# Performance work log

Measured on AMD Instinct MI355X. Metric: run time of the kernel, lower is better.

Reference implementation:

```python
import jax, jax.numpy as jnp
import numpy as np

N = 16384      # tokens
D_IN = 256     # input feature dim
D = 1024       # d_model
H = 2048       # expert hidden dim (2 * d_model)
E = 8          # n_experts
K = 2          # top_k
OUT = 2        # output classes
EPS = 1e-5


def layernorm(x, g, b):
    m = jnp.mean(x, axis=-1, keepdims=True)
    v = jnp.mean(jnp.square(x - m), axis=-1, keepdims=True)
    return (x - m) * jax.lax.rsqrt(v + EPS) * g + b


def setup_inputs() -> dict:
    key = jax.random.key(0)
    ks = jax.random.split(key, 10)
    s_in = 1.0 / np.sqrt(D_IN)
    s_d = 1.0 / np.sqrt(D)
    s_h = 1.0 / np.sqrt(H)
    return {
        "x": jax.random.normal(ks[0], (N, D_IN), jnp.float32),
        "w_in": jax.random.normal(ks[1], (D_IN, D), jnp.float32) * s_in,
        "b_in": jnp.zeros((D,), jnp.float32),
        "g_in": jnp.ones((D,), jnp.float32),
        "beta_in": jnp.zeros((D,), jnp.float32),
        "w_gate": jax.random.normal(ks[2], (D, E), jnp.float32) * s_d,
        "w1": jax.random.normal(ks[3], (E, D, H), jnp.float32) * s_d,
        "b1": jnp.zeros((E, H), jnp.float32),
        "w2": jax.random.normal(ks[4], (E, H, D), jnp.float32) * s_h,
        "b2": jnp.zeros((E, D), jnp.float32),
        "g_moe": jnp.ones((D,), jnp.float32),
        "beta_moe": jnp.zeros((D,), jnp.float32),
        "g_out": jnp.ones((D,), jnp.float32),
        "beta_out": jnp.zeros((D,), jnp.float32),
        "w_cls": jax.random.normal(ks[5], (D, OUT), jnp.float32) * s_d,
        "b_cls": jnp.zeros((OUT,), jnp.float32),
    }


def reference(x, w_in, b_in, g_in, beta_in, w_gate, w1, b1, w2, b2,
              g_moe, beta_moe, g_out, beta_out, w_cls, b_cls):
    # input projection + norm
    h = layernorm(x @ w_in + b_in, g_in, beta_in)            # [N, D]
    # router: softmax then top-k, renormalize over selected experts
    probs = jax.nn.softmax(h @ w_gate, axis=-1)              # [N, E]
    _, top_idx = jax.lax.top_k(probs, K)                     # [N, K]
    sel = jax.nn.one_hot(top_idx, E, dtype=probs.dtype).sum(axis=1)  # [N, E] 0/1
    gates = probs * sel
    gates = gates / (jnp.sum(gates, axis=-1, keepdims=True) + 1e-9)
    # experts: weighted combine; gate==0 tokens contribute nothing (same math
    # as the torch masked gather/scatter-add, dropout off in eval)
    mixed = jnp.zeros_like(h)
    for e in range(E):  # fixed, small expert count
        expert_out = jax.nn.gelu(h @ w1[e] + b1[e]) @ w2[e] + b2[e]  # [N, D]
        mixed = mixed + gates[:, e:e + 1] * expert_out
    out = layernorm(h + mixed, g_moe, beta_moe)
    out = layernorm(out, g_out, beta_out)
    return out @ w_cls + b_cls                               # [N, OUT]
```

## Files before the change

### kernel.cpp

```cpp
#include <hip/hip_runtime.h>
#include <hip/hip_bf16.h>

#define D_IN 256
#define DM   1024
#define HD   2048
#define NE   8
#define NTOK 16384

typedef __attribute__((ext_vector_type(8))) short short8;
typedef __attribute__((ext_vector_type(4))) float f32x4;
typedef unsigned int uint;

#define MT_TOFF1 0
#define MT_TOFF2 512
#define MT_CNT1  1536
#define MT_P1    1600
#define MT_OFF1  1664
#define MT_CNT2  1728
#define MT_PCNT2 1856
#define MT_TOTAL 1984

__device__ inline ushort f2bf(float v){
  __hip_bfloat16 b = __float2bfloat16(v);
  return *reinterpret_cast<ushort*>(&b);
}
__device__ inline float bf2f(ushort u){
  __hip_bfloat16 b = *reinterpret_cast<__hip_bfloat16*>(&u);
  return __bfloat162float(b);
}

__device__ inline float gelu_fast(float x){
  float u = 0.7978845608028654f * x * (1.0f + 0.044715f*x*x);
  return x / (1.0f + __expf(-2.0f*u));
}

__device__ inline void gload16(const void* g, void* l){
  __builtin_amdgcn_global_load_lds(
      (const __attribute__((address_space(1))) void*)g,
      (__attribute__((address_space(3))) void*)l, 16, 0, 0);
}


__global__ __launch_bounds__(256) void transpose_bf16_kernel(
    const float* __restrict__ src, ushort* __restrict__ dst, int R, int C)
{
  __shared__ float tile[32][33];
  int e = blockIdx.z;
  src += (size_t)e*R*C; dst += (size_t)e*R*C;
  int c0 = blockIdx.x*32, r0 = blockIdx.y*32;
  int tx = threadIdx.x & 31, ty = threadIdx.x >> 5;
  #pragma unroll
  for (int rr = ty; rr < 32; rr += 8)
    tile[rr][tx] = src[(size_t)(r0+rr)*C + c0+tx];
  __syncthreads();
  #pragma unroll
  for (int rr = ty; rr < 32; rr += 8)
    dst[(size_t)(c0+rr)*R + r0+tx] = f2bf(tile[tx][rr]);
}

__global__ __launch_bounds__(256) void split_x_kernel(
    const float* __restrict__ x, ushort* __restrict__ xs3)
{
  int g = blockIdx.x*256 + threadIdx.x;
  int e0 = g*4;
  int row = e0 >> 8, col = e0 & 255;
  f32x4 v = *(const f32x4*)(x + (size_t)row*D_IN + col);
  ushort4 hi, mi, lo;
  #pragma unroll
  for (int i=0;i<4;++i){
    float f = v[i];
    ushort h = f2bf(f);       float fh = bf2f(h);
    ushort m = f2bf(f - fh);  float fm = bf2f(m);
    ushort l = f2bf(f - fh - fm);
    ((ushort*)&hi)[i]=h; ((ushort*)&mi)[i]=m; ((ushort*)&lo)[i]=l;
  }
  ushort* base = xs3 + (size_t)row*768 + col;
  *(ushort4*)(base)       = hi;
  *(ushort4*)(base + 256) = mi;
  *(ushort4*)(base + 512) = lo;
}

__global__ __launch_bounds__(256) void transpose_split3_kernel(
    const float* __restrict__ src, ushort* __restrict__ dst)
{
  __shared__ float tile[32][33];
  int c0 = blockIdx.x*32, r0 = blockIdx.y*32;
  int tx = threadIdx.x & 31, ty = threadIdx.x >> 5;
  #pragma unroll
  for (int rr = ty; rr < 32; rr += 8)
    tile[rr][tx] = src[(size_t)(r0+rr)*DM + c0+tx];
  __syncthreads();
  #pragma unroll
  for (int rr = ty; rr < 32; rr += 8){
    float f = tile[tx][rr];
    ushort h = f2bf(f);       float fh = bf2f(h);
    ushort m = f2bf(f - fh);  float fm = bf2f(m);
    ushort l = f2bf(f - fh - fm);
    ushort* d = dst + (size_t)(c0+rr)*768 + r0 + tx;
    d[0]   = h;
    d[256] = m;
    d[512] = l;
  }
}

__global__ __launch_bounds__(256) void wgate_t_kernel(
    const float* __restrict__ w_gate, float* __restrict__ wgt)
{
  int e = blockIdx.x;
  for (int j = threadIdx.x; j < DM; j += 256)
    wgt[(size_t)e*DM + j] = w_gate[(size_t)j*NE + e];
}

__global__ __launch_bounds__(256) void gemm_router(
    const ushort* __restrict__ A,
    const ushort* __restrict__ BT,
    const float* __restrict__ b_in,
    float* __restrict__ y)
{
  __shared__ ushort As[3][128*32];
  __shared__ ushort Bs[3][128*32];
  const int tid = threadIdx.x;
  const int w = tid>>6, l = tid&63;
  const int wm = w>>1, wn = w&1;
  const int bm0 = blockIdx.y*128, bn0 = blockIdx.x*128;
  const int lr = l&15, lk = l>>4;
  const int rsub = l>>2;
  const int csub = ((l&3) ^ ((l>>3)&3)) * 8;

  const ushort* ag[2]; const ushort* bg[2];
  int aslot[2];
  #pragma unroll
  for (int i=0;i<2;++i){
    int ra = bm0 + w*32 + i*16 + rsub;
    int rb = bn0 + w*32 + i*16 + rsub;
    ag[i] = A  + (size_t)ra*768 + csub;
    bg[i] = BT + (size_t)rb*768 + csub;
    aslot[i] = (w*32 + i*16)*32;
  }

  const int pOffT[6] = {0,256,0,256,512,0};
  const int qOffT[6] = {0,0,256,256,0,512};
  auto stage = [&](int db, int t){
    int pOff = pOffT[t>>3] + (t&7)*32;
    int qOff = qOffT[t>>3] + (t&7)*32;
    #pragma unroll
    for (int i=0;i<2;++i){
      gload16(ag[i]+pOff, (ushort*)As[db] + aslot[i]);
      gload16(bg[i]+qOff, (ushort*)Bs[db] + aslot[i]);
    }
  };

  f32x4 acc[4][4] = {};
  const int NK = 48;
  stage(0, 0); stage(1, 1);
  int cur = 0;
  for (int t=0; t<NK; ++t){
    int sb = cur - 1; if (sb < 0) sb = 2;
    if (t+2 < NK)     { stage(sb, t+2); asm volatile("s_waitcnt vmcnt(8)" ::: "memory"); }
    else if (t+1 < NK){                 asm volatile("s_waitcnt vmcnt(4)" ::: "memory"); }
    else              {                 asm volatile("s_waitcnt vmcnt(0)" ::: "memory"); }
    __builtin_amdgcn_s_barrier();
    short8 af[4], bf[4];
    #pragma unroll
    for (int i=0;i<4;++i)
      af[i] = *(const short8*)(As[cur] + (wm*64 + i*16 + lr)*32 + (lk ^ ((lr>>1)&3))*8);
    #pragma unroll
    for (int j=0;j<4;++j)
      bf[j] = *(const short8*)(Bs[cur] + (wn*64 + j*16 + lr)*32 + (lk ^ ((lr>>1)&3))*8);
    #pragma unroll
    for (int i=0;i<4;++i){
      #pragma unroll
      for (int j=0;j<4;++j)
        acc[i][j] = __builtin_amdgcn_mfma_f32_16x16x32_bf16(af[i], bf[j], acc[i][j], 0, 0, 0);
    }
    __builtin_amdgcn_s_barrier();
    cur = cur + 1; if (cur > 2) cur = 0;
  }

  #pragma unroll
  for (int i=0;i<4;++i){
    #pragma unroll
    for (int j=0;j<4;++j){
      int n = bn0 + wn*64 + j*16 + lr;
      float bn_ = b_in[n];
      #pragma unroll
      for (int r=0;r<4;++r){
        int m = bm0 + wm*64 + i*16 + lk*4 + r;
        y[(size_t)m*DM + n] = acc[i][j][r] + bn_;
      }
    }
  }
}

__device__ inline double wredd(double v){
  #pragma unroll
  for (int o=32;o>0;o>>=1) v += __shfl_xor(v, o, 64);
  return v;
}

__global__ __launch_bounds__(256) void ln_router_kernel(
    const float* __restrict__ g_in, const float* __restrict__ beta_in,
    const float* __restrict__ wgt,
    ushort* __restrict__ hbf, float* __restrict__ resid,
    float* __restrict__ gates, int* __restrict__ selmask)
{
  int tok = blockIdx.x*4 + (threadIdx.x>>6);
  int l = threadIdx.x & 63;
  float* row = resid + (size_t)tok*DM;
  float u[16];
  double s=0.0, q=0.0;
  #pragma unroll
  for (int r=0;r<16;++r){ u[r]=row[l+64*r]; s+=u[r]; q+=(double)u[r]*u[r]; }
  s = wredd(s); q = wredd(q);
  double mean = s*(1.0/1024.0);
  double var  = q*(1.0/1024.0) - mean*mean;
  double rstd = 1.0/sqrt(var + 1e-5);

  double lg[NE];
  #pragma unroll
  for (int e=0;e<NE;++e) lg[e]=0.0;
  float hv[16];
  #pragma unroll
  for (int r=0;r<16;++r){
    int j = l + 64*r;
    double v = ((double)u[r]-mean)*rstd*(double)g_in[j] + (double)beta_in[j];
    hv[r] = (float)v;
    #pragma unroll
    for (int e=0;e<NE;++e) lg[e] += v*(double)wgt[(size_t)e*DM + j];
  }
  #pragma unroll
  for (int r=0;r<16;++r){
    int j = l + 64*r;
    row[j] = hv[r];
    hbf[(size_t)tok*DM + j] = f2bf(hv[r]);
  }
  #pragma unroll
  for (int e=0;e<NE;++e) lg[e] = wredd(lg[e]);

  if (l==0){
    double mx = lg[0];
    #pragma unroll
    for (int e=1;e<NE;++e) mx = lg[e]>mx ? lg[e] : mx;
    double p[NE]; double sum=0.0;
    #pragma unroll
    for (int e=0;e<NE;++e){ p[e]=exp(lg[e]-mx); sum+=p[e]; }
    #pragma unroll
    for (int e=0;e<NE;++e) p[e]/=sum;
    int i1=0;
    for (int e=1;e<NE;++e) if (p[e]>p[i1]) i1=e;
    int i2=-1;
    for (int e=0;e<NE;++e){ if (e==i1) continue; if (i2<0 || p[e]>p[i2]) i2=e; }
    double denom = p[i1]+p[i2]+1e-9;
    float g[NE];
    #pragma unroll
    for (int e=0;e<NE;++e) g[e]=0.f;
    g[i1]=(float)(p[i1]/denom);
    g[i2]=(float)(p[i2]/denom);
    #pragma unroll
    for (int e=0;e<NE;++e) gates[(size_t)tok*NE+e]=g[e];
    selmask[tok] = (1<<i1)|(1<<i2);
  }
}

__global__ __launch_bounds__(256) void builder_count(
    const int* __restrict__ selmask, uint* __restrict__ bc1, uint* __restrict__ bc2)
{
  __shared__ uint c1[8], c2s[16];
  int b = blockIdx.x, tid = threadIdx.x;
  if (tid<8) c1[tid]=0;
  if (tid<16) c2s[tid]=0;
  __syncthreads();
  int m = selmask[b*256+tid];
  int ea = __ffs(m)-1, eb = 31-__clz(m);
  atomicAdd(&c1[ea],1u); atomicAdd(&c1[eb],1u);
  atomicAdd(&c2s[ea],1u); atomicAdd(&c2s[8+eb],1u);
  __syncthreads();
  if (tid<8) bc1[b*8+tid]=c1[tid];
  if (tid<16) bc2[b*16+tid]=c2s[tid];
}

__global__ __launch_bounds__(256) void builder_scan(
    const uint* __restrict__ bc1, const uint* __restrict__ bc2,
    uint* __restrict__ meta, int nch, int TPC)
{
  int tid = threadIdx.x;
  int c = tid/24, k = tid%24;
  if (c < nch){
    if (k < 8){
      uint run=0;
      for (int b=c*TPC; b<(c+1)*TPC; ++b){ meta[MT_TOFF1 + b*8 + k] = run; run += bc1[b*8+k]; }
      meta[MT_CNT1 + c*8 + k] = run;
    } else {
      int k2 = k-8;
      uint run=0;
      for (int b=c*TPC; b<(c+1)*TPC; ++b){ meta[MT_TOFF2 + b*16 + k2] = run; run += bc2[b*16+k2]; }
      meta[MT_CNT2 + c*16 + k2] = run;
      meta[MT_PCNT2 + c*16 + k2] = ((run + 127u)/128u)*128u;
    }
  }
  __syncthreads();
  if (tid < nch){
    uint off=0;
    for (int e=0;e<8;++e){
      uint cn = meta[MT_CNT1 + tid*8 + e];
      uint p = ((cn+127u)/128u)*128u;
      meta[MT_P1 + tid*8 + e] = p;
      meta[MT_OFF1 + tid*8 + e] = off;
      off += p;
    }
  }
}

__device__ inline int exclscan256(int v, int* sc, int tid){
  sc[tid]=v; __syncthreads();
  #pragma unroll
  for (int o=1;o<256;o<<=1){
    int x = (tid>=o) ? sc[tid-o] : 0;
    __syncthreads();
    sc[tid]+=x;
    __syncthreads();
  }
  int incl = sc[tid]; __syncthreads();
  return incl - v;
}

__global__ __launch_bounds__(256) void builder_fill(
    const int* __restrict__ selmask, const uint* __restrict__ meta,
    int* __restrict__ ids1, int CH)
{
  __shared__ int sc[256];
  int b = blockIdx.x, tid = threadIdx.x;
  int t = b*256 + tid;
  int c = t / CH;
  int m = selmask[t];
  int ea = __ffs(m)-1, eb = 31-__clz(m);
  int ja=0, jb=0;
  for (int e=0;e<8;++e){
    int r0 = exclscan256((ea==e)?1:0, sc, tid);
    if (ea==e) ja = r0;
    int r1 = exclscan256((eb==e)?1:0, sc, tid);
    if (eb==e) jb = r1;
  }
  {
    uint j    = meta[MT_TOFF2 + b*16 + ea] + (uint)ja;
    ids1[(c*8+ea)*CH + j] = t;
  }
  {
    uint j    = meta[MT_TOFF2 + b*16 + 8 + eb] + (uint)jb;
    uint pos1 = meta[MT_CNT2 + c*16 + eb] + j;
    ids1[(c*8+eb)*CH + pos1] = t;
  }
}

__global__ __launch_bounds__(256) void gemm_ffn1(
    const ushort* __restrict__ Abase,
    const ushort* __restrict__ BT,
    const int*   __restrict__ rows,
    const uint*  __restrict__ pcnt,
    const uint*  __restrict__ off1,
    const float* __restrict__ bias,
    ushort* __restrict__ t1,
    int K, int N, int CH)
{
  const int e = blockIdx.z;
  const int bm0 = blockIdx.y*128;
  if ((uint)bm0 >= pcnt[e]) return;
  const int bn0 = blockIdx.x*128;

  __shared__ ushort As[3][128*32];
  __shared__ ushort Bs[3][128*32];
  const int tid = threadIdx.x;
  const int w = tid>>6, l = tid&63;
  const int wm = w>>1, wn = w&1;
  const int lr = l&15, lk = l>>4;
  const int rsub = l>>2;
  const int csub = ((l&3) ^ ((l>>3)&3)) * 8;

  const ushort* ag[2]; const ushort* bg[2];
  int slot[2];
  #pragma unroll
  for (int i=0;i<2;++i){
    int ra = w*32 + i*16 + rsub;
    int id = rows[e*CH + bm0 + ra];
    ag[i] = Abase + (size_t)id*K + csub;
    int rb = bn0 + w*32 + i*16 + rsub;
    bg[i] = BT + (size_t)e*N*K + (size_t)rb*K + csub;
    slot[i] = (w*32 + i*16)*32;
  }

  auto stage = [&](int db, int kt){
    #pragma unroll
    for (int i=0;i<2;++i){
      gload16(ag[i]+kt, (ushort*)As[db] + slot[i]);
      gload16(bg[i]+kt, (ushort*)Bs[db] + slot[i]);
    }
  };

  f32x4 acc[4][4] = {};
  const int NK = K>>5;
  stage(0, 0); stage(1, 32);
  int cur = 0;
  for (int t=0; t<NK; ++t){
    int sb = cur - 1; if (sb < 0) sb = 2;
    if (t+2 < NK)     { stage(sb, (t+2)<<5); asm volatile("s_waitcnt vmcnt(8)" ::: "memory"); }
    else if (t+1 < NK){                      asm volatile("s_waitcnt vmcnt(4)" ::: "memory"); }
    else              {                      asm volatile("s_waitcnt vmcnt(0)" ::: "memory"); }
    __builtin_amdgcn_s_barrier();
    short8 af[4], bf[4];
    #pragma unroll
    for (int i=0;i<4;++i)
      af[i] = *(const short8*)(As[cur] + (wm*64 + i*16 + lr)*32 + (lk ^ ((lr>>1)&3))*8);
    #pragma unroll
    for (int j=0;j<4;++j)
      bf[j] = *(const short8*)(Bs[cur] + (wn*64 + j*16 + lr)*32 + (lk ^ ((lr>>1)&3))*8);
    #pragma unroll
    for (int i=0;i<4;++i){
      #pragma unroll
      for (int j=0;j<4;++j)
        acc[i][j] = __builtin_amdgcn_mfma_f32_16x16x32_bf16(af[i], bf[j], acc[i][j], 0, 0, 0);
    }
    __builtin_amdgcn_s_barrier();
    cur = cur + 1; if (cur > 2) cur = 0;
  }

  #pragma unroll
  for (int i=0;i<4;++i){
    #pragma unroll
    for (int j=0;j<4;++j){
      int n = bn0 + wn*64 + j*16 + lr;
      float bn_ = bias[(size_t)e*N + n];
      #pragma unroll
      for (int r=0;r<4;++r){
        int mloc = wm*64 + i*16 + lk*4 + r;
        float v = acc[i][j][r] + bn_;
        size_t trow = (size_t)off1[e] + bm0 + mloc;
        t1[trow*N + n] = f2bf(gelu_fast(v));
      }
    }
  }
}

template<int SLOT>
__global__ __launch_bounds__(256) void gemm_ffn2(
    const ushort* __restrict__ t1,
    const ushort* __restrict__ BT,
    const int*   __restrict__ ids1,
    const uint*  __restrict__ cnt2,
    const uint*  __restrict__ pcnt2,
    const uint*  __restrict__ off1,
    const float* __restrict__ bias,
    const float* __restrict__ gates,
    float* __restrict__ resid,
    int K, int N, int CH)
{
  const int e = blockIdx.z;
  const int bm0 = blockIdx.y*128;
  if ((uint)bm0 >= pcnt2[SLOT*8 + e]) return;
  const uint scnt  = cnt2[SLOT*8 + e];
  const uint start = (SLOT==1) ? cnt2[e] : 0u;
  const int bn0 = blockIdx.x*128;

  __shared__ ushort As[3][128*32];
  __shared__ ushort Bs[3][128*32];
  const int tid = threadIdx.x;
  const int w = tid>>6, l = tid&63;
  const int wm = w>>1, wn = w&1;
  const int lr = l&15, lk = l>>4;
  const int rsub = l>>2;
  const int csub = ((l&3) ^ ((l>>3)&3)) * 8;

  const ushort* ag[2]; const ushort* bg[2];
  int slot[2];
  #pragma unroll
  for (int i=0;i<2;++i){
    int ra = w*32 + i*16 + rsub;
    size_t arow = (size_t)off1[e] + start + bm0 + ra;
    ag[i] = t1 + arow*K + csub;
    int rb = bn0 + w*32 + i*16 + rsub;
    bg[i] = BT + (size_t)e*N*K + (size_t)rb*K + csub;
    slot[i] = (w*32 + i*16)*32;
  }

  auto stage = [&](int db, int kt){
    #pragma unroll
    for (int i=0;i<2;++i){
      gload16(ag[i]+kt, (ushort*)As[db] + slot[i]);
      gload16(bg[i]+kt, (ushort*)Bs[db] + slot[i]);
    }
  };

  f32x4 acc[4][4] = {};
  const int NK = K>>5;
  stage(0, 0); stage(1, 32);
  int cur = 0;
  for (int t=0; t<NK; ++t){
    int sb = cur - 1; if (sb < 0) sb = 2;
    if (t+2 < NK)     { stage(sb, (t+2)<<5); asm volatile("s_waitcnt vmcnt(8)" ::: "memory"); }
    else if (t+1 < NK){                      asm volatile("s_waitcnt vmcnt(4)" ::: "memory"); }
    else              {                      asm volatile("s_waitcnt vmcnt(0)" ::: "memory"); }
    __builtin_amdgcn_s_barrier();
    short8 af[4], bf[4];
    #pragma unroll
    for (int i=0;i<4;++i)
      af[i] = *(const short8*)(As[cur] + (wm*64 + i*16 + lr)*32 + (lk ^ ((lr>>1)&3))*8);
    #pragma unroll
    for (int j=0;j<4;++j)
      bf[j] = *(const short8*)(Bs[cur] + (wn*64 + j*16 + lr)*32 + (lk ^ ((lr>>1)&3))*8);
    #pragma unroll
    for (int i=0;i<4;++i){
      #pragma unroll
      for (int j=0;j<4;++j)
        acc[i][j] = __builtin_amdgcn_mfma_f32_16x16x32_bf16(af[i], bf[j], acc[i][j], 0, 0, 0);
    }
    __builtin_amdgcn_s_barrier();
    cur = cur + 1; if (cur > 2) cur = 0;
  }

  #pragma unroll
  for (int i=0;i<4;++i){
    #pragma unroll
    for (int j=0;j<4;++j){
      int n = bn0 + wn*64 + j*16 + lr;
      float bn_ = bias[(size_t)e*N + n];
      #pragma unroll
      for (int r=0;r<4;++r){
        int mloc = wm*64 + i*16 + lk*4 + r;
        int mg = bm0 + mloc;
        if ((uint)mg < scnt){
          int tok = ids1[e*CH + (int)start + mg];
          float g = gates[(size_t)tok*NE + e];
          resid[(size_t)tok*N + n] += g*(acc[i][j][r] + bn_);
        }
      }
    }
  }
}

__global__ __launch_bounds__(256) void final_kernel(
    const float* __restrict__ resid,
    const float* __restrict__ g_moe, const float* __restrict__ beta_moe,
    const float* __restrict__ g_out, const float* __restrict__ beta_out,
    const float* __restrict__ w_cls, const float* __restrict__ b_cls,
    float* __restrict__ out)
{
  int tok = blockIdx.x*4 + (threadIdx.x>>6);
  int l = threadIdx.x & 63;
  const float* row = resid + (size_t)tok*DM;
  float u[16];
  double s=0.0,q=0.0;
  #pragma unroll
  for (int r=0;r<16;++r){ u[r]=row[l + 64*r]; s+=u[r]; q+=(double)u[r]*u[r]; }
  s=wredd(s); q=wredd(q);
  double m1 = s*(1.0/1024.0), v1 = q*(1.0/1024.0)-m1*m1;
  double rs1 = 1.0/sqrt(v1+1e-5);
  float tv[16]; double s2=0.0,q2=0.0;
  #pragma unroll
  for (int r=0;r<16;++r){
    int j = l+64*r;
    float vv = (float)((u[r]-m1)*rs1)*g_moe[j] + beta_moe[j];
    tv[r]=vv; s2+=vv; q2+=(double)vv*vv;
  }
  s2=wredd(s2); q2=wredd(q2);
  double m2=s2*(1.0/1024.0), v2=q2*(1.0/1024.0)-m2*m2;
  double rs2=1.0/sqrt(v2+1e-5);
  double p0=0.0,p1=0.0;
  #pragma unroll
  for (int r=0;r<16;++r){
    int j=l+64*r;
    double y=((double)tv[r]-m2)*rs2*(double)g_out[j]+(double)beta_out[j];
    p0+=y*(double)w_cls[j*2]; p1+=y*(double)w_cls[j*2+1];
  }
  p0=wredd(p0); p1=wredd(p1);
  if (l==0){
    out[(size_t)tok*2  ]=(float)(p0+(double)b_cls[0]);
    out[(size_t)tok*2+1]=(float)(p1+(double)b_cls[1]);
  }
}

extern "C" void kernel_launch(void* const* d_in, const int* in_sizes, int n_in,
                              void* d_out, int out_size, void* d_ws, size_t ws_size,
                              hipStream_t stream)
{
  (void)in_sizes; (void)n_in; (void)out_size;
  const float* x       = (const float*)d_in[0];
  const float* w_in    = (const float*)d_in[1];
  const float* b_in    = (const float*)d_in[2];
  const float* g_in    = (const float*)d_in[3];
  const float* beta_in = (const float*)d_in[4];
  const float* w_gate  = (const float*)d_in[5];
  const float* w1      = (const float*)d_in[6];
  const float* b1      = (const float*)d_in[7];
  const float* w2      = (const float*)d_in[8];
  const float* b2      = (const float*)d_in[9];
  const float* g_moe   = (const float*)d_in[10];
  const float* beta_mo = (const float*)d_in[11];
  const float* g_out   = (const float*)d_in[12];
  const float* beta_ou = (const float*)d_in[13];
  const float* w_cls   = (const float*)d_in[14];
  const float* b_cls   = (const float*)d_in[15];
  float* out = (float*)d_out;

  char* p = (char*)d_ws;
  ushort* w1t   = (ushort*)p; p += (size_t)NE*HD*DM*2;
  ushort* w2t   = (ushort*)p; p += (size_t)NE*DM*HD*2;
  ushort* hbf   = (ushort*)p; p += (size_t)NTOK*DM*2;
  float*  resid = (float*)p;  p += (size_t)NTOK*DM*4;
  float*  gates = (float*)p;  p += (size_t)NTOK*NE*4;
  int*    selmk = (int*)p;    p += (size_t)NTOK*4;
  int*    ids1  = (int*)p;    p += (size_t)NE*NTOK*4;
  ushort* wt3   = (ushort*)p; p += (size_t)DM*768*2;
  float*  wgt   = (float*)p;  p += (size_t)NE*DM*4;
  uint*   bc1   = (uint*)p;   p += (size_t)64*8*4;
  uint*   bc2   = (uint*)p;   p += (size_t)64*16*4;
  uint*   meta  = (uint*)p;   p += (size_t)MT_TOTAL*4;
  size_t fixed = (size_t)(p - (char*)d_ws);

  const size_t xs3_bytes = (size_t)NTOK*768*2;
  size_t t1b1 = ((size_t)2*NTOK        + 2048)*HD*2;
  size_t t1b2 = ((size_t)2*(NTOK/2)    + 2048)*HD*2;
  size_t t1b4 = ((size_t)2*(NTOK/4)    + 2048)*HD*2;
  int nch = 8;
  if      (ws_size >= fixed + (t1b1 > xs3_bytes ? t1b1 : xs3_bytes)) nch = 1;
  else if (ws_size >= fixed + (t1b2 > xs3_bytes ? t1b2 : xs3_bytes)) nch = 2;
  else if (ws_size >= fixed + (t1b4 > xs3_bytes ? t1b4 : xs3_bytes)) nch = 4;
  const int CH  = NTOK/nch;
  const int TPC = CH/256;
  ushort* t1  = (ushort*)p;
  ushort* xs3 = (ushort*)p;

  split_x_kernel<<<dim3(NTOK*D_IN/4/256), 256, 0, stream>>>(x, xs3);
  transpose_split3_kernel<<<dim3(DM/32, D_IN/32), 256, 0, stream>>>(w_in, wt3);
  wgate_t_kernel<<<dim3(NE), 256, 0, stream>>>(w_gate, wgt);
  transpose_bf16_kernel<<<dim3(HD/32, DM/32, NE), 256, 0, stream>>>(w1, w1t, DM, HD);
  transpose_bf16_kernel<<<dim3(DM/32, HD/32, NE), 256, 0, stream>>>(w2, w2t, HD, DM);

  gemm_router<<<dim3(DM/128, NTOK/128), 256, 0, stream>>>(xs3, wt3, b_in, resid);
  ln_router_kernel<<<dim3(NTOK/4), 256, 0, stream>>>(g_in, beta_in, wgt,
                                                     hbf, resid, gates, selmk);

  hipMemsetAsync(ids1, 0, (size_t)NE*NTOK*4, stream);

  builder_count<<<dim3(NTOK/256), 256, 0, stream>>>(selmk, bc1, bc2);
  builder_scan<<<dim3(1), 256, 0, stream>>>(bc1, bc2, meta, nch, TPC);
  builder_fill<<<dim3(NTOK/256), 256, 0, stream>>>(selmk, meta, ids1, CH);

  for (int c = 0; c < nch; ++c) {
    gemm_ffn1<<<dim3(HD/128, CH/128, NE), 256, 0, stream>>>(
        hbf, w1t, ids1 + (size_t)c*8*CH,
        meta+MT_P1+c*8, meta+MT_OFF1+c*8, b1, t1, DM, HD, CH);
    gemm_ffn2<0><<<dim3(DM/128, CH/128, NE), 256, 0, stream>>>(
        t1, w2t, ids1 + (size_t)c*8*CH,
        meta+MT_CNT2+c*16, meta+MT_PCNT2+c*16, meta+MT_OFF1+c*8,
        b2, gates, resid, HD, DM, CH);
    gemm_ffn2<1><<<dim3(DM/128, CH/128, NE), 256, 0, stream>>>(
        t1, w2t, ids1 + (size_t)c*8*CH,
        meta+MT_CNT2+c*16, meta+MT_PCNT2+c*16, meta+MT_OFF1+c*8,
        b2, gates, resid, HD, DM, CH);
  }

  final_kernel<<<dim3(NTOK/4), 256, 0, stream>>>(resid, g_moe, beta_mo, g_out, beta_ou,
                                                 w_cls, b_cls, out);
}
```

Before: 892.0 us.

## Enlarge FFN1 tile to 256x128 with 512 threads and raise MFMA priority

The expert FFN1 GEMM now computes a 256-row by 128-column tile per block using 8 waves, so each weight tile loaded into LDS is reused across twice as many token rows and the gathered A rows are staged in a single coalesced pass. Expert row padding is raised from 128 to 256, and the t1 workspace sizing is adjusted to match. s_setprio is placed around the MFMA loops in all three GEMMs to favour matrix issue over loads from other waves. The trade-offs are more padded rows per expert, larger LDS use per block that may lower occupancy, and a different chunk-count threshold.

```diff
diff --git a/kernel.cpp b/kernel.cpp
--- a/kernel.cpp
+++ b/kernel.cpp
@@ -167,12 +167,14 @@
     #pragma unroll
     for (int j=0;j<4;++j)
       bf[j] = *(const short8*)(Bs[cur] + (wn*64 + j*16 + lr)*32 + (lk ^ ((lr>>1)&3))*8);
+    __builtin_amdgcn_s_setprio(1);
     #pragma unroll
     for (int i=0;i<4;++i){
       #pragma unroll
       for (int j=0;j<4;++j)
         acc[i][j] = __builtin_amdgcn_mfma_f32_16x16x32_bf16(af[i], bf[j], acc[i][j], 0, 0, 0);
     }
+    __builtin_amdgcn_s_setprio(0);
     __builtin_amdgcn_s_barrier();
     cur = cur + 1; if (cur > 2) cur = 0;
   }
@@ -303,7 +305,7 @@
     uint off=0;
     for (int e=0;e<8;++e){
       uint cn = meta[MT_CNT1 + tid*8 + e];
-      uint p = ((cn+127u)/128u)*128u;
+      uint p = ((cn+255u)/256u)*256u;
       meta[MT_P1 + tid*8 + e] = p;
       meta[MT_OFF1 + tid*8 + e] = off;
       off += p;
@@ -352,7 +354,7 @@
   }
 }
 
-__global__ __launch_bounds__(256) void gemm_ffn1(
+__global__ __launch_bounds__(512) void gemm_ffn1(
     const ushort* __restrict__ Abase,
     const ushort* __restrict__ BT,
     const int*   __restrict__ rows,
@@ -363,37 +365,33 @@
     int K, int N, int CH)
 {
   const int e = blockIdx.z;
-  const int bm0 = blockIdx.y*128;
+  const int bm0 = blockIdx.y*256;
   if ((uint)bm0 >= pcnt[e]) return;
   const int bn0 = blockIdx.x*128;
 
-  __shared__ ushort As[3][128*32];
+  __shared__ ushort As[3][256*32];
   __shared__ ushort Bs[3][128*32];
   const int tid = threadIdx.x;
-  const int w = tid>>6, l = tid&63;
-  const int wm = w>>1, wn = w&1;
+  const int wid = tid>>6, l = tid&63;
+  const int wm = wid>>1, wn = wid&1;
   const int lr = l&15, lk = l>>4;
-  const int rsub = l>>2;
-  const int csub = ((l&3) ^ ((l>>3)&3)) * 8;
-
-  const ushort* ag[2]; const ushort* bg[2];
-  int slot[2];
-  #pragma unroll
-  for (int i=0;i<2;++i){
-    int ra = w*32 + i*16 + rsub;
-    int id = rows[e*CH + bm0 + ra];
-    ag[i] = Abase + (size_t)id*K + csub;
-    int rb = bn0 + w*32 + i*16 + rsub;
-    bg[i] = BT + (size_t)e*N*K + (size_t)rb*K + csub;
-    slot[i] = (w*32 + i*16)*32;
+
+  const ushort* agp[2]; const ushort* bgp;
+  #pragma unroll
+  for (int pss=0;pss<2;++pss){
+    int rowa = (pss*512 + tid)>>2;
+    int id = rows[e*CH + bm0 + rowa];
+    agp[pss] = Abase + (size_t)id*K + (((tid&3) ^ ((rowa>>1)&3))*8);
+  }
+  {
+    int rowb = tid>>2;
+    bgp = BT + (size_t)e*N*K + (size_t)(bn0 + rowb)*K + (((tid&3) ^ ((rowb>>1)&3))*8);
   }
 
   auto stage = [&](int db, int kt){
-    #pragma unroll
-    for (int i=0;i<2;++i){
-      gload16(ag[i]+kt, (ushort*)As[db] + slot[i]);
-      gload16(bg[i]+kt, (ushort*)Bs[db] + slot[i]);
-    }
+    gload16(agp[0]+kt, (ushort*)As[db] + tid*8);
+    gload16(agp[1]+kt, (ushort*)As[db] + (512+tid)*8);
+    gload16(bgp   +kt, (ushort*)Bs[db] + tid*8);
   };
 
   f32x4 acc[4][4] = {};
@@ -402,23 +400,29 @@
   int cur = 0;
   for (int t=0; t<NK; ++t){
     int sb = cur - 1; if (sb < 0) sb = 2;
-    if (t+2 < NK)     { stage(sb, (t+2)<<5); asm volatile("s_waitcnt vmcnt(8)" ::: "memory"); }
-    else if (t+1 < NK){                      asm volatile("s_waitcnt vmcnt(4)" ::: "memory"); }
+    if (t+2 < NK)     { stage(sb, (t+2)<<5); asm volatile("s_waitcnt vmcnt(6)" ::: "memory"); }
+    else if (t+1 < NK){                      asm volatile("s_waitcnt vmcnt(3)" ::: "memory"); }
     else              {                      asm volatile("s_waitcnt vmcnt(0)" ::: "memory"); }
     __builtin_amdgcn_s_barrier();
     short8 af[4], bf[4];
     #pragma unroll
-    for (int i=0;i<4;++i)
-      af[i] = *(const short8*)(As[cur] + (wm*64 + i*16 + lr)*32 + (lk ^ ((lr>>1)&3))*8);
-    #pragma unroll
-    for (int j=0;j<4;++j)
-      bf[j] = *(const short8*)(Bs[cur] + (wn*64 + j*16 + lr)*32 + (lk ^ ((lr>>1)&3))*8);
+    for (int i=0;i<4;++i){
+      int r = wm*64 + i*16 + lr;
+      af[i] = *(const short8*)(As[cur] + r*32 + (lk ^ ((r>>1)&3))*8);
+    }
+    #pragma unroll
+    for (int j=0;j<4;++j){
+      int rb = wn*64 + j*16 + lr;
+      bf[j] = *(const short8*)(Bs[cur] + rb*32 + (lk ^ ((rb>>1)&3))*8);
+    }
+    __builtin_amdgcn_s_setprio(1);
     #pragma unroll
     for (int i=0;i<4;++i){
       #pragma unroll
       for (int j=0;j<4;++j)
         acc[i][j] = __builtin_amdgcn_mfma_f32_16x16x32_bf16(af[i], bf[j], acc[i][j], 0, 0, 0);
     }
+    __builtin_amdgcn_s_setprio(0);
     __builtin_amdgcn_s_barrier();
     cur = cur + 1; if (cur > 2) cur = 0;
   }
@@ -506,12 +510,14 @@
     #pragma unroll
     for (int j=0;j<4;++j)
       bf[j] = *(const short8*)(Bs[cur] + (wn*64 + j*16 + lr)*32 + (lk ^ ((lr>>1)&3))*8);
+    __builtin_amdgcn_s_setprio(1);
     #pragma unroll
     for (int i=0;i<4;++i){
       #pragma unroll
       for (int j=0;j<4;++j)
         acc[i][j] = __builtin_amdgcn_mfma_f32_16x16x32_bf16(af[i], bf[j], acc[i][j], 0, 0, 0);
     }
+    __builtin_amdgcn_s_setprio(0);
     __builtin_amdgcn_s_barrier();
     cur = cur + 1; if (cur > 2) cur = 0;
   }
@@ -616,9 +622,9 @@
   size_t fixed = (size_t)(p - (char*)d_ws);
 
   const size_t xs3_bytes = (size_t)NTOK*768*2;
-  size_t t1b1 = ((size_t)2*NTOK        + 2048)*HD*2;
-  size_t t1b2 = ((size_t)2*(NTOK/2)    + 2048)*HD*2;
-  size_t t1b4 = ((size_t)2*(NTOK/4)    + 2048)*HD*2;
+  size_t t1b1 = ((size_t)2*NTOK        + 2304)*HD*2;
+  size_t t1b2 = ((size_t)2*(NTOK/2)    + 2304)*HD*2;
+  size_t t1b4 = ((size_t)2*(NTOK/4)    + 2304)*HD*2;
   int nch = 8;
   if      (ws_size >= fixed + (t1b1 > xs3_bytes ? t1b1 : xs3_bytes)) nch = 1;
   else if (ws_size >= fixed + (t1b2 > xs3_bytes ? t1b2 : xs3_bytes)) nch = 2;
@@ -645,7 +651,7 @@
   builder_fill<<<dim3(NTOK/256), 256, 0, stream>>>(selmk, meta, ids1, CH);
 
   for (int c = 0; c < nch; ++c) {
-    gemm_ffn1<<<dim3(HD/128, CH/128, NE), 256, 0, stream>>>(
+    gemm_ffn1<<<dim3(HD/128, CH/256, NE), 512, 0, stream>>>(
         hbf, w1t, ids1 + (size_t)c*8*CH,
         meta+MT_P1+c*8, meta+MT_OFF1+c*8, b1, t1, DM, HD, CH);
     gemm_ffn2<0><<<dim3(DM/128, CH/128, NE), 256, 0, stream>>>(
```

New measurement: 904.0 us. About the same (+1.3%).
